# Optimization experiments

Hardware: AMD Instinct MI355X
Metric: run time of the kernel (lower is better)

Reference implementation:

```python
import jax, jax.numpy as jnp
import numpy as np

N_NODES = 50000
N_EDGES = 600000
HID = 128
N_LAYERS = 3
NEG_SLOPE = 0.01  # torch.nn.LeakyReLU default


def setup_inputs() -> dict:
    key = jax.random.key(0)
    ks = jax.random.split(key, 7)
    x = jax.random.normal(ks[0], (N_NODES, HID), dtype=jnp.float32)
    edge_index = jax.random.randint(ks[1], (2, N_EDGES), 0, N_NODES, dtype=jnp.int64)
    edge_attr = jax.random.normal(ks[2], (N_EDGES, 2), dtype=jnp.float32)
    # GINEConv edge projection Linear(edge_dim=2 -> in_channels=128), stacked over layers
    Wl = jax.random.normal(ks[3], (N_LAYERS, 2, HID), dtype=jnp.float32) * 0.1
    bl = jax.random.normal(ks[4], (N_LAYERS, HID), dtype=jnp.float32) * 0.1
    # GINEConv update nn = Linear(128 -> 128), stacked over layers
    W = jax.random.normal(ks[5], (N_LAYERS, HID, HID), dtype=jnp.float32) * (1.0 / np.sqrt(HID))
    b = jax.random.normal(ks[6], (N_LAYERS, HID), dtype=jnp.float32) * 0.1
    return {"x": x, "edge_index": edge_index, "edge_attr": edge_attr,
            "Wl": Wl, "bl": bl, "W": W, "b": b}


def reference(x, edge_index, edge_attr, Wl, bl, W, b):
    # PyG flow source_to_target: edge_index[0]=src j, edge_index[1]=dst i
    src, dst = edge_index[0], edge_index[1]
    n = x.shape[0]
    h = x
    for i in range(N_LAYERS):
        e = edge_attr @ Wl[i] + bl[i]                      # [E, HID] edge projection
        msg = jax.nn.relu(h[src] + e)                      # gather + fuse edge feats
        agg = jax.ops.segment_sum(msg, dst, num_segments=n)  # scatter-add to targets
        h = ((1.0 + 0.0) * h + agg) @ W[i] + b[i]          # eps = 0 (GINEConv default)
        h = jnp.where(h >= 0, h, NEG_SLOPE * h)            # LeakyReLU
    return h
```

## Files before the change

kernel.cpp:

```cpp
#include <hip/hip_runtime.h>

#define NNODES 50000
#define NEDGES 600000
#define HID 128
#define NLAYERS 3
#define NEG 0.01f
#define SCAN_B ((NNODES + 1023) / 1024)
#define FILL_BPG 150
#define CVT_B 12500
#define ZERO_B 196
#define WCONV_B 24
#define NPB 16

typedef __attribute__((ext_vector_type(8))) short short8;
typedef __attribute__((ext_vector_type(4))) float f32x4;

__device__ __forceinline__ unsigned int f2bf(float f) {
    unsigned int u = __float_as_uint(f);
    return (u + 0x7fffu + ((u >> 16) & 1u)) >> 16;
}
__device__ __forceinline__ float bf2f(unsigned int h) {
    return __uint_as_float(h << 16);
}
__device__ __forceinline__ float bflo(unsigned int p) { return __uint_as_float(p << 16); }
__device__ __forceinline__ float bfhi(unsigned int p) { return __uint_as_float(p & 0xffff0000u); }

__global__ __launch_bounds__(256) void prep_k(const float* __restrict__ x,
                                              unsigned int* __restrict__ hb,
                                              int* __restrict__ off,
                                              const float* __restrict__ W,
                                              uint4* __restrict__ whf,
                                              uint4* __restrict__ wlf) {
    const int b = blockIdx.x;
    const int t = threadIdx.x;
    if (b < CVT_B) {
        const int i = b * 256 + t;
        const float2 v = *(const float2*)(x + (size_t)i * 2);
        hb[i] = f2bf(v.x) | (f2bf(v.y) << 16);
    } else if (b < CVT_B + ZERO_B) {
        const int i = (b - CVT_B) * 256 + t;
        if (i <= NNODES) off[i] = 0;
    } else {
        const int g = ((b - CVT_B - ZERO_B) * 256 + t) >> 6;
        if (g >= NLAYERS * 32) return;
        const int lane = t & 63;
        const int l = g >> 5;
        const int kt = (g >> 3) & 3;
        const int nt = g & 7;
        const int n = nt * 16 + (lane & 15);
        const int k0 = kt * 32 + (lane >> 4) * 8;
        unsigned int hh[8], ll[8];
#pragma unroll
        for (int j = 0; j < 8; ++j) {
            const float w = W[l * HID * HID + (k0 + j) * HID + n];
            const unsigned int wh = f2bf(w);
            hh[j] = wh;
            ll[j] = f2bf(w - bf2f(wh));
        }
        uint4 ph, pl;
        ph.x = hh[0] | (hh[1] << 16); ph.y = hh[2] | (hh[3] << 16);
        ph.z = hh[4] | (hh[5] << 16); ph.w = hh[6] | (hh[7] << 16);
        pl.x = ll[0] | (ll[1] << 16); pl.y = ll[2] | (ll[3] << 16);
        pl.z = ll[4] | (ll[5] << 16); pl.w = ll[6] | (ll[7] << 16);
        const int idx = ((l * 4 + kt) * 8 + nt) * 64 + lane;
        whf[idx] = ph;
        wlf[idx] = pl;
    }
}


__global__ __launch_bounds__(256) void hist_k(const int* __restrict__ ei,
                                              int* __restrict__ deg) {
    const int e = blockIdx.x * blockDim.x + threadIdx.x;
    if (e < NEDGES) atomicAdd(&deg[ei[NEDGES + e]], 1);
}

__global__ __launch_bounds__(1024) void scan1_k(const int* __restrict__ deg,
                                                int* __restrict__ part,
                                                int* __restrict__ bsum) {
    __shared__ int s[1024];
    const int t = threadIdx.x;
    const int i = blockIdx.x * 1024 + t;
    const int v = (i < NNODES) ? deg[i] : 0;
    s[t] = v;
    __syncthreads();
    for (int d = 1; d < 1024; d <<= 1) {
        const int add = (t >= d) ? s[t - d] : 0;
        __syncthreads();
        s[t] += add;
        __syncthreads();
    }
    if (i < NNODES) part[i] = s[t] - v;
    if (t == 1023) bsum[blockIdx.x] = s[1023];
}

__global__ __launch_bounds__(1024) void scan2_k(const int* __restrict__ part,
                                                const int* __restrict__ bsum,
                                                int* __restrict__ off,
                                                int* __restrict__ cur) {
    const int b = blockIdx.x;
    const int t = threadIdx.x;
    const int lane = t & 63;
    int v = (lane < b) ? bsum[lane] : 0;
#pragma unroll
    for (int d = 1; d < 64; d <<= 1) v += __shfl_xor(v, d);
    const int i = b * 1024 + t;
    if (i < NNODES) {
        const int e = part[i] + v;
        off[i] = e;
        cur[i] = e;
    }
    if (b == 0 && t == 0) off[NNODES] = NEDGES;
}

__global__ __launch_bounds__(256) void fill_k(const int* __restrict__ ei,
                                              const float* __restrict__ ea,
                                              int* __restrict__ cur,
                                              unsigned long long* __restrict__ meta) {
    const int g = blockIdx.x & 7;
    const int bg = blockIdx.x >> 3;
    const int dlo = g * (NNODES / 8);
    const int dhi = dlo + (NNODES / 8);
    const int stride = FILL_BPG * 256;
    for (int e = bg * 256 + threadIdx.x; e < NEDGES; e += stride) {
        const int d = ei[NEDGES + e];
        if (d >= dlo && d < dhi) {
            const int s = ei[e];
            const float2 av = *(const float2*)(ea + 2 * e);
            const int p = atomicAdd(&cur[d], 1);
            meta[p] = (unsigned long long)(unsigned int)s |
                      ((unsigned long long)(f2bf(av.x) | (f2bf(av.y) << 16)) << 32);
        }
    }
}

__global__ __launch_bounds__(256) void layer_k(
    const unsigned int* __restrict__ hb,
    const unsigned long long* __restrict__ meta,
    const float* __restrict__ Wl,
    const float* __restrict__ bl,
    const int* __restrict__ off,
    const uint4* __restrict__ whf,
    const uint4* __restrict__ wlf,
    const float* __restrict__ bias,
    float* __restrict__ out,
    unsigned short* __restrict__ hbo,
    const int last)
{
    __shared__ unsigned int vsh[NPB * 68];
    const int tid = threadIdx.x;
    const int wave = tid >> 6;
    const int lane = tid & 63;
    const int nb = blockIdx.x * NPB;

    const int f0 = lane << 1;
    const float2 w0 = *(const float2*)(Wl + f0);
    const float2 w1 = *(const float2*)(Wl + HID + f0);
    const float2 bb = *(const float2*)(bl + f0);
    for (int i = 0; i < 4; ++i) {
        const int nl = wave * 4 + i;
        const int node = nb + nl;
        const unsigned int hp = hb[(size_t)node * 64 + lane];
        float2 acc = make_float2(bflo(hp), bfhi(hp));
        int idx = off[node];
        const int e1 = off[node + 1];
        for (; idx + 8 <= e1; idx += 8) {
            unsigned long long m[8];
#pragma unroll
            for (int j = 0; j < 8; ++j) m[j] = meta[idx + j];
            unsigned int g[8];
#pragma unroll
            for (int j = 0; j < 8; ++j)
                g[j] = hb[(size_t)(unsigned int)m[j] * 64 + lane];
#pragma unroll
            for (int j = 0; j < 8; ++j) {
                const unsigned int ap = (unsigned int)(m[j] >> 32);
                const float a0 = bflo(ap), a1 = bfhi(ap);
                acc.x += fmaxf(bflo(g[j]) + fmaf(a0, w0.x, fmaf(a1, w1.x, bb.x)), 0.f);
                acc.y += fmaxf(bfhi(g[j]) + fmaf(a0, w0.y, fmaf(a1, w1.y, bb.y)), 0.f);
            }
        }
        if (idx + 4 <= e1) {
            unsigned long long m[4];
#pragma unroll
            for (int j = 0; j < 4; ++j) m[j] = meta[idx + j];
            unsigned int g[4];
#pragma unroll
            for (int j = 0; j < 4; ++j)
                g[j] = hb[(size_t)(unsigned int)m[j] * 64 + lane];
#pragma unroll
            for (int j = 0; j < 4; ++j) {
                const unsigned int ap = (unsigned int)(m[j] >> 32);
                const float a0 = bflo(ap), a1 = bfhi(ap);
                acc.x += fmaxf(bflo(g[j]) + fmaf(a0, w0.x, fmaf(a1, w1.x, bb.x)), 0.f);
                acc.y += fmaxf(bfhi(g[j]) + fmaf(a0, w0.y, fmaf(a1, w1.y, bb.y)), 0.f);
            }
            idx += 4;
        }
        for (; idx < e1; ++idx) {
            const unsigned long long m = meta[idx];
            const unsigned int g = hb[(size_t)(unsigned int)m * 64 + lane];
            const unsigned int ap = (unsigned int)(m >> 32);
            const float a0 = bflo(ap), a1 = bfhi(ap);
            acc.x += fmaxf(bflo(g) + fmaf(a0, w0.x, fmaf(a1, w1.x, bb.x)), 0.f);
            acc.y += fmaxf(bfhi(g) + fmaf(a0, w0.y, fmaf(a1, w1.y, bb.y)), 0.f);
        }
        vsh[nl * 68 + lane] = f2bf(acc.x) | (f2bf(acc.y) << 16);
    }
    __syncthreads();

    const int lrow = lane & 15;
    short8 a[4];
#pragma unroll
    for (int kt = 0; kt < 4; ++kt) {
        const uint4 t = *(const uint4*)&vsh[lrow * 68 + (kt * 4 + (lane >> 4)) * 4];
        a[kt] = *(const short8*)&t;
    }
    const int crow0 = nb + (lane >> 4) * 4;
    const int ncol = lane & 15;
#pragma unroll
    for (int ntl = 0; ntl < 2; ++ntl) {
        const int nt = wave * 2 + ntl;
        const float bv = bias[nt * 16 + ncol];
        f32x4 acc = {bv, bv, bv, bv};
#pragma unroll
        for (int kt = 0; kt < 4; ++kt) {
            uint4 th = whf[(kt * 8 + nt) * 64 + lane];
            uint4 tl = wlf[(kt * 8 + nt) * 64 + lane];
            acc = __builtin_amdgcn_mfma_f32_16x16x32_bf16(a[kt], *(short8*)&th, acc, 0, 0, 0);
            acc = __builtin_amdgcn_mfma_f32_16x16x32_bf16(a[kt], *(short8*)&tl, acc, 0, 0, 0);
        }
#pragma unroll
        for (int r = 0; r < 4; ++r) {
            const int rr = crow0 + r;
            float v = acc[r];
            v = v >= 0.f ? v : NEG * v;
            if (last) out[(size_t)rr * HID + nt * 16 + ncol] = v;
            else      hbo[(size_t)rr * HID + nt * 16 + ncol] = (unsigned short)f2bf(v);
        }
    }
}

extern "C" void kernel_launch(void* const* d_in, const int* in_sizes, int n_in,
                              void* d_out, int out_size, void* d_ws, size_t ws_size,
                              hipStream_t stream) {
    const float* x  = (const float*)d_in[0];
    const int*   ei = (const int*)d_in[1];
    const float* ea = (const float*)d_in[2];
    const float* Wl = (const float*)d_in[3];
    const float* bl = (const float*)d_in[4];
    const float* W  = (const float*)d_in[5];
    const float* b  = (const float*)d_in[6];

    float* h = (float*)d_out;

    unsigned long long* meta = (unsigned long long*)d_ws;
    unsigned int* hb0 = (unsigned int*)(meta + NEDGES);
    unsigned int* hb1 = hb0 + (size_t)NNODES * 64;
    uint4* whf = (uint4*)(hb1 + (size_t)NNODES * 64);
    uint4* wlf = whf + NLAYERS * 4 * 8 * 64;
    int* off  = (int*)(wlf + NLAYERS * 4 * 8 * 64);
    int* cur  = off + NNODES + 1;
    int* part = cur + NNODES;
    int* bsum = part + NNODES;

    prep_k<<<CVT_B + ZERO_B + WCONV_B, 256, 0, stream>>>(x, hb0, off, W, whf, wlf);
    hist_k<<<(NEDGES + 255) / 256, 256, 0, stream>>>(ei, off);
    scan1_k<<<SCAN_B, 1024, 0, stream>>>(off, part, bsum);
    scan2_k<<<SCAN_B, 1024, 0, stream>>>(part, bsum, off, cur);
    fill_k<<<8 * FILL_BPG, 256, 0, stream>>>(ei, ea, cur, meta);

    unsigned int* hin = hb0;
    unsigned int* hout = hb1;
    for (int l = 0; l < NLAYERS; ++l) {
        layer_k<<<NNODES / NPB, 256, 0, stream>>>(
            hin, meta, Wl + (size_t)l * 2 * HID, bl + (size_t)l * HID, off,
            whf + (size_t)l * 4 * 8 * 64, wlf + (size_t)l * 4 * 8 * 64,
            b + (size_t)l * HID, h, (unsigned short*)hout, l == NLAYERS - 1);
        unsigned int* tmp = hin; hin = hout; hout = tmp;
    }
}
```

Before: 194.0 us.

## Flatten per-wave edge loop across four nodes with software-prefetched metadata

```diff
diff --git a/kernel.cpp b/kernel.cpp
--- a/kernel.cpp
+++ b/kernel.cpp
@@ -147,65 +147,78 @@
     unsigned short* __restrict__ hbo,
     const int last)
 {
+    __shared__ float lacc[4][4][64][2];
     __shared__ unsigned int vsh[NPB * 68];
     const int tid = threadIdx.x;
     const int wave = tid >> 6;
     const int lane = tid & 63;
     const int nb = blockIdx.x * NPB;
+    const int n0 = nb + wave * 4;
 
     const int f0 = lane << 1;
     const float2 w0 = *(const float2*)(Wl + f0);
     const float2 w1 = *(const float2*)(Wl + HID + f0);
     const float2 bb = *(const float2*)(bl + f0);
+
+#pragma unroll
+    for (int i = 0; i < 4; ++i) {
+        const unsigned int hp = hb[(size_t)(n0 + i) * 64 + lane];
+        lacc[wave][i][lane][0] = bflo(hp);
+        lacc[wave][i][lane][1] = bfhi(hp);
+    }
+
+    const int o0 = off[n0];
+    const int o1 = off[n0 + 1];
+    const int o2 = off[n0 + 2];
+    const int o3 = off[n0 + 3];
+    const int o4 = off[n0 + 4];
+
+    if (o0 < o4) {
+        unsigned long long m[8];
+#pragma unroll
+        for (int j = 0; j < 8; ++j)
+            m[j] = meta[min(o0 + j, o4 - 1)];
+        float raccx = 0.f, raccy = 0.f;
+        int dcur = 0;
+        for (int idx = o0; idx < o4; idx += 8) {
+            unsigned int g[8];
+#pragma unroll
+            for (int j = 0; j < 8; ++j)
+                g[j] = hb[(size_t)(unsigned int)m[j] * 64 + lane];
+            const int nxt = idx + 8;
+            unsigned long long m2[8];
+#pragma unroll
+            for (int j = 0; j < 8; ++j)
+                m2[j] = (nxt < o4) ? meta[min(nxt + j, o4 - 1)] : 0ull;
+#pragma unroll
+            for (int j = 0; j < 8; ++j) {
+                const int e = idx + j;
+                if (e < o4) {
+                    const int dl = (e >= o1) + (e >= o2) + (e >= o3);
+                    if (dl != dcur) {
+                        lacc[wave][dcur][lane][0] += raccx;
+                        lacc[wave][dcur][lane][1] += raccy;
+                        raccx = 0.f; raccy = 0.f;
+                        dcur = dl;
+                    }
+                    const unsigned int ap = (unsigned int)(m[j] >> 32);
+                    const float a0 = bflo(ap), a1 = bfhi(ap);
+                    raccx += fmaxf(bflo(g[j]) + fmaf(a0, w0.x, fmaf(a1, w1.x, bb.x)), 0.f);
+                    raccy += fmaxf(bfhi(g[j]) + fmaf(a0, w0.y, fmaf(a1, w1.y, bb.y)), 0.f);
+                }
+            }
+#pragma unroll
+            for (int j = 0; j < 8; ++j) m[j] = m2[j];
+        }
+        lacc[wave][dcur][lane][0] += raccx;
+        lacc[wave][dcur][lane][1] += raccy;
+    }
+
+#pragma unroll
     for (int i = 0; i < 4; ++i) {
         const int nl = wave * 4 + i;
-        const int node = nb + nl;
-        const unsigned int hp = hb[(size_t)node * 64 + lane];
-        float2 acc = make_float2(bflo(hp), bfhi(hp));
-        int idx = off[node];
-        const int e1 = off[node + 1];
-        for (; idx + 8 <= e1; idx += 8) {
-            unsigned long long m[8];
-#pragma unroll
-            for (int j = 0; j < 8; ++j) m[j] = meta[idx + j];
-            unsigned int g[8];
-#pragma unroll
-            for (int j = 0; j < 8; ++j)
-                g[j] = hb[(size_t)(unsigned int)m[j] * 64 + lane];
-#pragma unroll
-            for (int j = 0; j < 8; ++j) {
-                const unsigned int ap = (unsigned int)(m[j] >> 32);
-                const float a0 = bflo(ap), a1 = bfhi(ap);
-                acc.x += fmaxf(bflo(g[j]) + fmaf(a0, w0.x, fmaf(a1, w1.x, bb.x)), 0.f);
-                acc.y += fmaxf(bfhi(g[j]) + fmaf(a0, w0.y, fmaf(a1, w1.y, bb.y)), 0.f);
-            }
-        }
-        if (idx + 4 <= e1) {
-            unsigned long long m[4];
-#pragma unroll
-            for (int j = 0; j < 4; ++j) m[j] = meta[idx + j];
-            unsigned int g[4];
-#pragma unroll
-            for (int j = 0; j < 4; ++j)
-                g[j] = hb[(size_t)(unsigned int)m[j] * 64 + lane];
-#pragma unroll
-            for (int j = 0; j < 4; ++j) {
-                const unsigned int ap = (unsigned int)(m[j] >> 32);
-                const float a0 = bflo(ap), a1 = bfhi(ap);
-                acc.x += fmaxf(bflo(g[j]) + fmaf(a0, w0.x, fmaf(a1, w1.x, bb.x)), 0.f);
-                acc.y += fmaxf(bfhi(g[j]) + fmaf(a0, w0.y, fmaf(a1, w1.y, bb.y)), 0.f);
-            }
-            idx += 4;
-        }
-        for (; idx < e1; ++idx) {
-            const unsigned long long m = meta[idx];
-            const unsigned int g = hb[(size_t)(unsigned int)m * 64 + lane];
-            const unsigned int ap = (unsigned int)(m >> 32);
-            const float a0 = bflo(ap), a1 = bfhi(ap);
-            acc.x += fmaxf(bflo(g) + fmaf(a0, w0.x, fmaf(a1, w1.x, bb.x)), 0.f);
-            acc.y += fmaxf(bfhi(g) + fmaf(a0, w0.y, fmaf(a1, w1.y, bb.y)), 0.f);
-        }
-        vsh[nl * 68 + lane] = f2bf(acc.x) | (f2bf(acc.y) << 16);
+        vsh[nl * 68 + lane] =
+            f2bf(lacc[wave][i][lane][0]) | (f2bf(lacc[wave][i][lane][1]) << 16);
     }
     __syncthreads();
 
```

Result: slower. 210.0 us (+8.3%).

## Split layer into sliced-feature aggregation and separate GEMM kernels

Applied to the files above, without the earlier changes.

```diff
diff --git a/kernel.cpp b/kernel.cpp
--- a/kernel.cpp
+++ b/kernel.cpp
@@ -10,7 +10,9 @@
 #define CVT_B 12500
 #define ZERO_B 196
 #define WCONV_B 24
-#define NPB 16
+#define NPB2 48
+#define AGG_NB ((NNODES + NPB2 - 1) / NPB2)
+#define MCAP2 1024
 
 typedef __attribute__((ext_vector_type(8))) short short8;
 typedef __attribute__((ext_vector_type(4))) float f32x4;
@@ -35,8 +37,13 @@
     const int t = threadIdx.x;
     if (b < CVT_B) {
         const int i = b * 256 + t;
-        const float2 v = *(const float2*)(x + (size_t)i * 2);
-        hb[i] = f2bf(v.x) | (f2bf(v.y) << 16);
+        const int node = i >> 6;
+        const int fp = i & 63;
+        const int slice = fp >> 3;
+        const int fl = fp & 7;
+        const float2 v = *(const float2*)(x + (size_t)node * HID + fp * 2);
+        hb[(size_t)slice * NNODES * 8 + (size_t)node * 8 + fl] =
+            f2bf(v.x) | (f2bf(v.y) << 16);
     } else if (b < CVT_B + ZERO_B) {
         const int i = (b - CVT_B) * 256 + t;
         if (i <= NNODES) off[i] = 0;
@@ -134,12 +141,68 @@
     }
 }
 
-__global__ __launch_bounds__(256) void layer_k(
+__global__ __launch_bounds__(256) void agg_k(
     const unsigned int* __restrict__ hb,
     const unsigned long long* __restrict__ meta,
     const float* __restrict__ Wl,
     const float* __restrict__ bl,
     const int* __restrict__ off,
+    unsigned int* __restrict__ vh)
+{
+    __shared__ unsigned long long msh[MCAP2];
+    const int tid = threadIdx.x;
+    const int slice = blockIdx.x & 7;
+    const int bg = blockIdx.x >> 3;
+    const int nb = bg * NPB2;
+    const int nhi = min(nb + NPB2, NNODES);
+    const int mbeg = off[nb];
+    const int cnt = off[nhi] - mbeg;
+    for (int i = tid; i < cnt && i < MCAP2; i += 256)
+        msh[i] = meta[mbeg + i];
+
+    const int lane = tid & 63;
+    const int wave = tid >> 6;
+    const int fl = lane & 7;
+    const int eo = lane >> 3;
+    const int f0 = slice * 16 + fl * 2;
+    const float2 w0 = *(const float2*)(Wl + f0);
+    const float2 w1 = *(const float2*)(Wl + HID + f0);
+    const float2 bb = *(const float2*)(bl + f0);
+    const unsigned int* hbs = hb + (size_t)slice * NNODES * 8;
+    unsigned int* vhs = vh + (size_t)slice * NNODES * 8;
+    const bool lds_ok = (cnt <= MCAP2);
+    __syncthreads();
+
+    for (int i = 0; i < NPB2 / 4; ++i) {
+        const int node = nb + wave * (NPB2 / 4) + i;
+        if (node >= NNODES) break;
+        const int e0 = off[node], e1 = off[node + 1];
+        const unsigned int hp = hbs[(size_t)node * 8 + fl];
+        float ax = 0.f, ay = 0.f;
+        for (int base = e0; base < e1; base += 8) {
+            const int eidx = base + eo;
+            const bool valid = eidx < e1;
+            const unsigned long long m = lds_ok
+                ? msh[(valid ? eidx : e0) - mbeg]
+                : meta[valid ? eidx : e0];
+            const unsigned int g = hbs[(size_t)(unsigned int)m * 8 + fl];
+            const unsigned int ap = (unsigned int)(m >> 32);
+            const float a0 = bflo(ap), a1 = bfhi(ap);
+            const float mx = fmaxf(bflo(g) + fmaf(a0, w0.x, fmaf(a1, w1.x, bb.x)), 0.f);
+            const float my = fmaxf(bfhi(g) + fmaf(a0, w0.y, fmaf(a1, w1.y, bb.y)), 0.f);
+            if (valid) { ax += mx; ay += my; }
+        }
+        ax += __shfl_xor(ax, 8);  ay += __shfl_xor(ay, 8);
+        ax += __shfl_xor(ax, 16); ay += __shfl_xor(ay, 16);
+        ax += __shfl_xor(ax, 32); ay += __shfl_xor(ay, 32);
+        ax += bflo(hp);           ay += bfhi(hp);
+        if (lane < 8)
+            vhs[(size_t)node * 8 + fl] = f2bf(ax) | (f2bf(ay) << 16);
+    }
+}
+
+__global__ __launch_bounds__(256) void gemm_k(
+    const unsigned int* __restrict__ vh,
     const uint4* __restrict__ whf,
     const uint4* __restrict__ wlf,
     const float* __restrict__ bias,
@@ -147,80 +210,27 @@
     unsigned short* __restrict__ hbo,
     const int last)
 {
-    __shared__ unsigned int vsh[NPB * 68];
     const int tid = threadIdx.x;
     const int wave = tid >> 6;
     const int lane = tid & 63;
-    const int nb = blockIdx.x * NPB;
-
-    const int f0 = lane << 1;
-    const float2 w0 = *(const float2*)(Wl + f0);
-    const float2 w1 = *(const float2*)(Wl + HID + f0);
-    const float2 bb = *(const float2*)(bl + f0);
-    for (int i = 0; i < 4; ++i) {
-        const int nl = wave * 4 + i;
-        const int node = nb + nl;
-        const unsigned int hp = hb[(size_t)node * 64 + lane];
-        float2 acc = make_float2(bflo(hp), bfhi(hp));
-        int idx = off[node];
-        const int e1 = off[node + 1];
-        for (; idx + 8 <= e1; idx += 8) {
-            unsigned long long m[8];
-#pragma unroll
-            for (int j = 0; j < 8; ++j) m[j] = meta[idx + j];
-            unsigned int g[8];
-#pragma unroll
-            for (int j = 0; j < 8; ++j)
-                g[j] = hb[(size_t)(unsigned int)m[j] * 64 + lane];
-#pragma unroll
-            for (int j = 0; j < 8; ++j) {
-                const unsigned int ap = (unsigned int)(m[j] >> 32);
-                const float a0 = bflo(ap), a1 = bfhi(ap);
-                acc.x += fmaxf(bflo(g[j]) + fmaf(a0, w0.x, fmaf(a1, w1.x, bb.x)), 0.f);
-                acc.y += fmaxf(bfhi(g[j]) + fmaf(a0, w0.y, fmaf(a1, w1.y, bb.y)), 0.f);
-            }
-        }
-        if (idx + 4 <= e1) {
-            unsigned long long m[4];
-#pragma unroll
-            for (int j = 0; j < 4; ++j) m[j] = meta[idx + j];
-            unsigned int g[4];
-#pragma unroll
-            for (int j = 0; j < 4; ++j)
-                g[j] = hb[(size_t)(unsigned int)m[j] * 64 + lane];
-#pragma unroll
-            for (int j = 0; j < 4; ++j) {
-                const unsigned int ap = (unsigned int)(m[j] >> 32);
-                const float a0 = bflo(ap), a1 = bfhi(ap);
-                acc.x += fmaxf(bflo(g[j]) + fmaf(a0, w0.x, fmaf(a1, w1.x, bb.x)), 0.f);
-                acc.y += fmaxf(bfhi(g[j]) + fmaf(a0, w0.y, fmaf(a1, w1.y, bb.y)), 0.f);
-            }
-            idx += 4;
-        }
-        for (; idx < e1; ++idx) {
-            const unsigned long long m = meta[idx];
-            const unsigned int g = hb[(size_t)(unsigned int)m * 64 + lane];
-            const unsigned int ap = (unsigned int)(m >> 32);
-            const float a0 = bflo(ap), a1 = bfhi(ap);
-            acc.x += fmaxf(bflo(g) + fmaf(a0, w0.x, fmaf(a1, w1.x, bb.x)), 0.f);
-            acc.y += fmaxf(bfhi(g) + fmaf(a0, w0.y, fmaf(a1, w1.y, bb.y)), 0.f);
-        }
-        vsh[nl * 68 + lane] = f2bf(acc.x) | (f2bf(acc.y) << 16);
-    }
-    __syncthreads();
-
-    const int lrow = lane & 15;
+    const int rowbase = blockIdx.x * 64 + wave * 16;
+    const int arow = rowbase + (lane & 15);
+    const int arowc = arow < NNODES ? arow : NNODES - 1;
+    const int q = lane >> 4;
+
     short8 a[4];
 #pragma unroll
     for (int kt = 0; kt < 4; ++kt) {
-        const uint4 t = *(const uint4*)&vsh[lrow * 68 + (kt * 4 + (lane >> 4)) * 4];
+        const int slice = kt * 2 + (q >> 1);
+        const uint4 t = *(const uint4*)(vh + (size_t)slice * NNODES * 8 +
+                                        (size_t)arowc * 8 + (q & 1) * 4);
         a[kt] = *(const short8*)&t;
     }
-    const int crow0 = nb + (lane >> 4) * 4;
+
+    const int crow0 = rowbase + (lane >> 4) * 4;
     const int ncol = lane & 15;
 #pragma unroll
-    for (int ntl = 0; ntl < 2; ++ntl) {
-        const int nt = wave * 2 + ntl;
+    for (int nt = 0; nt < 8; ++nt) {
         const float bv = bias[nt * 16 + ncol];
         f32x4 acc = {bv, bv, bv, bv};
 #pragma unroll
@@ -233,10 +243,13 @@
 #pragma unroll
         for (int r = 0; r < 4; ++r) {
             const int rr = crow0 + r;
-            float v = acc[r];
-            v = v >= 0.f ? v : NEG * v;
-            if (last) out[(size_t)rr * HID + nt * 16 + ncol] = v;
-            else      hbo[(size_t)rr * HID + nt * 16 + ncol] = (unsigned short)f2bf(v);
+            if (rr < NNODES) {
+                float v = acc[r];
+                v = v >= 0.f ? v : NEG * v;
+                if (last) out[(size_t)rr * HID + nt * 16 + ncol] = v;
+                else      hbo[(size_t)nt * NNODES * 16 + (size_t)rr * 16 + ncol] =
+                              (unsigned short)f2bf(v);
+            }
         }
     }
 }
@@ -255,28 +268,26 @@
     float* h = (float*)d_out;
 
     unsigned long long* meta = (unsigned long long*)d_ws;
-    unsigned int* hb0 = (unsigned int*)(meta + NEDGES);
-    unsigned int* hb1 = hb0 + (size_t)NNODES * 64;
-    uint4* whf = (uint4*)(hb1 + (size_t)NNODES * 64);
+    unsigned int* vh = (unsigned int*)(meta + NEDGES);
+    unsigned int* hb = vh + (size_t)NNODES * 64;
+    uint4* whf = (uint4*)(hb + (size_t)NNODES * 64);
     uint4* wlf = whf + NLAYERS * 4 * 8 * 64;
     int* off  = (int*)(wlf + NLAYERS * 4 * 8 * 64);
     int* cur  = off + NNODES + 1;
     int* part = cur + NNODES;
     int* bsum = part + NNODES;
 
-    prep_k<<<CVT_B + ZERO_B + WCONV_B, 256, 0, stream>>>(x, hb0, off, W, whf, wlf);
+    prep_k<<<CVT_B + ZERO_B + WCONV_B, 256, 0, stream>>>(x, hb, off, W, whf, wlf);
     hist_k<<<(NEDGES + 255) / 256, 256, 0, stream>>>(ei, off);
     scan1_k<<<SCAN_B, 1024, 0, stream>>>(off, part, bsum);
     scan2_k<<<SCAN_B, 1024, 0, stream>>>(part, bsum, off, cur);
     fill_k<<<8 * FILL_BPG, 256, 0, stream>>>(ei, ea, cur, meta);
 
-    unsigned int* hin = hb0;
-    unsigned int* hout = hb1;
     for (int l = 0; l < NLAYERS; ++l) {
-        layer_k<<<NNODES / NPB, 256, 0, stream>>>(
-            hin, meta, Wl + (size_t)l * 2 * HID, bl + (size_t)l * HID, off,
-            whf + (size_t)l * 4 * 8 * 64, wlf + (size_t)l * 4 * 8 * 64,
-            b + (size_t)l * HID, h, (unsigned short*)hout, l == NLAYERS - 1);
-        unsigned int* tmp = hin; hin = hout; hout = tmp;
-    }
-}
+        agg_k<<<8 * AGG_NB, 256, 0, stream>>>(
+            hb, meta, Wl + (size_t)l * 2 * HID, bl + (size_t)l * HID, off, vh);
+        gemm_k<<<(NNODES + 63) / 64, 256, 0, stream>>>(
+            vh, whf + (size_t)l * 4 * 8 * 64, wlf + (size_t)l * 4 * 8 * 64,
+            b + (size_t)l * HID, h, (unsigned short*)hb, l == NLAYERS - 1);
+    }
+}
```

After: 353.8 us. 1.82x slower.
